# Optimization experiments

Measured on AMD Instinct MI355X. Metric: run time of the kernel, lower is better.

The kernel has to match this reference:

```python
import jax, jax.numpy as jnp
import numpy as np

NUM_HEADS = 16
HEAD_DIM = 64
NEG_INF = -1000000000.0


def rotary_embedding(x, seq_len, head_dim):
    # x: (batch, seq, heads, head_dim)
    positions = jnp.arange(seq_len)
    dim_pairs = jnp.arange(0, head_dim, 2)
    freqs = 1.0 / 10000.0 ** (dim_pairs / head_dim)
    angles = positions[:, None] * freqs[None, :]          # (seq, head_dim/2)
    cos = jnp.cos(angles)[:, None, :]                     # (seq, 1, head_dim/2) -> broadcast over heads
    sin = jnp.sin(angles)[:, None, :]
    x1 = x[..., ::2]
    x2 = x[..., 1::2]
    out1 = x1 * cos - x2 * sin
    out2 = x1 * sin + x2 * cos
    return jnp.stack([out1, out2], axis=-1).reshape(x.shape)


def setup_inputs() -> dict:
    key = jax.random.key(0)
    k1, k2, k3 = jax.random.split(key, 3)
    batch, seq_len, embed_dim = 2, 2048, 1024
    x = jax.random.normal(k1, (batch, seq_len, embed_dim), dtype=jnp.float32)
    W_qkv = jax.random.normal(k2, (embed_dim, 3 * NUM_HEADS * HEAD_DIM), dtype=jnp.float32) * 0.02
    W_out = jax.random.normal(k3, (NUM_HEADS * HEAD_DIM, embed_dim), dtype=jnp.float32) * 0.02
    return {"x": x, "W_qkv": W_qkv, "W_out": W_out}


def reference(x, W_qkv, W_out):
    batch, seq_len, embed_dim = x.shape
    qkv = jnp.einsum('bse,ef->bsf', x, W_qkv)
    qkv = qkv.reshape(batch, seq_len, 3, NUM_HEADS, HEAD_DIM)
    q, k, v = qkv[:, :, 0], qkv[:, :, 1], qkv[:, :, 2]
    q = rotary_embedding(q, seq_len, HEAD_DIM)
    k = rotary_embedding(k, seq_len, HEAD_DIM)
    scale = 1.0 / jnp.sqrt(jnp.asarray(HEAD_DIM, dtype=x.dtype))
    scores = jnp.einsum('bqhd,bkhd->bhqk', q, k) * scale   # (B,H,S,S)
    mask = jnp.tril(jnp.ones((seq_len, seq_len), dtype=bool))[None, None, :, :]
    scores = jnp.where(mask, scores, NEG_INF)
    weights = jax.nn.softmax(scores, axis=-1)
    out = jnp.einsum('bhqk,bkhd->bqhd', weights, v)
    out = out.reshape(batch, seq_len, NUM_HEADS * HEAD_DIM)
    return jnp.einsum('bsf,fe->bse', out, W_out)
```

## Files before the change

### kernel.cpp

```cpp
#include <hip/hip_runtime.h>
#include <hip/hip_bf16.h>

typedef __attribute__((ext_vector_type(8))) short short8;
typedef __attribute__((ext_vector_type(4))) float float4v;

__device__ inline short8 rope8(short8 raw, float4 tA, float4 tB, float scale) {
  float c[4] = {tA.x, tA.z, tB.x, tB.z};
  float s[4] = {tA.y, tA.w, tB.y, tB.w};
  union { short8 v; short e[8]; } in, out;
  in.v = raw;
  #pragma unroll
  for (int j = 0; j < 4; ++j) {
    __hip_bfloat16 h1 = *reinterpret_cast<__hip_bfloat16*>(&in.e[2 * j]);
    __hip_bfloat16 h2 = *reinterpret_cast<__hip_bfloat16*>(&in.e[2 * j + 1]);
    const float x1 = __bfloat162float(h1), x2 = __bfloat162float(h2);
    __hip_bfloat16 o1 = __float2bfloat16((x1 * c[j] - x2 * s[j]) * scale);
    __hip_bfloat16 o2 = __float2bfloat16((x1 * s[j] + x2 * c[j]) * scale);
    out.e[2 * j]     = *reinterpret_cast<short*>(&o1);
    out.e[2 * j + 1] = *reinterpret_cast<short*>(&o2);
  }
  return out.v;
}

__global__ __launch_bounds__(256) void prep_all(
    const float* __restrict__ x, __hip_bfloat16* __restrict__ xb,
    float2* __restrict__ tab,
    const float* __restrict__ Wqkv, const float* __restrict__ Wout,
    __hip_bfloat16* __restrict__ WqkvT, __hip_bfloat16* __restrict__ WoutT) {
  __shared__ __hip_bfloat16 tile[32][33];
  const int id = blockIdx.x;
  if (id < 4096) {
    const int i = id * 256 + threadIdx.x;
    const float4 v = *(const float4*)(x + (size_t)i * 4);
    __hip_bfloat16 o[4];
    o[0] = __float2bfloat16(v.x); o[1] = __float2bfloat16(v.y);
    o[2] = __float2bfloat16(v.z); o[3] = __float2bfloat16(v.w);
    *(uint2*)(xb + (size_t)i * 4) = *(const uint2*)o;
    return;
  }
  if (id < 4352) {
    const int i = (id - 4096) * 256 + threadIdx.x;
    const int s = i >> 5, p = i & 31;
    const float freq = powf(10000.f, -(float)(p * 2) / 64.f);
    float sn, cs;
    sincosf((float)s * freq, &sn, &cs);
    tab[i] = make_float2(cs, sn);
    return;
  }
  const float* in;
  __hip_bfloat16* out;
  int C, bx, by;
  if (id < 7424) {
    const int lid = id - 4352;
    in = Wqkv; out = WqkvT; C = 3072; bx = lid % 96; by = lid / 96;
  } else {
    const int lid = id - 7424;
    in = Wout; out = WoutT; C = 1024; bx = lid & 31; by = lid >> 5;
  }
  const int R = 1024;
  const int c0 = bx * 32, r0 = by * 32;
  const int tx = threadIdx.x & 31, ty = threadIdx.x >> 5;
  #pragma unroll
  for (int i = ty; i < 32; i += 8)
    tile[i][tx] = __float2bfloat16(in[(size_t)(r0 + i) * C + (c0 + tx)]);
  __syncthreads();
  const int sx = threadIdx.x & 15, sy = threadIdx.x >> 4;
  #pragma unroll
  for (int i = sy; i < 32; i += 16) {
    union { unsigned u; short e[2]; } pk;
    pk.e[0] = *reinterpret_cast<short*>(&tile[2 * sx][i]);
    pk.e[1] = *reinterpret_cast<short*>(&tile[2 * sx + 1][i]);
    *(unsigned*)&out[(size_t)(c0 + i) * R + r0 + 2 * sx] = pk.u;
  }
}

template <typename OutT, int BM, int BN>
__global__ __launch_bounds__(256) void gemm_bt(
    const __hip_bfloat16* __restrict__ A,
    const __hip_bfloat16* __restrict__ Bt,
    OutT* __restrict__ C,
    int M, int N, int K) {
  __shared__ __hip_bfloat16 lA[BM][64];
  __shared__ __hip_bfloat16 lB[BN][64];
  constexpr int NI = BM / 32, NJ = BN / 32;
  const int t = threadIdx.x;
  const int lane = t & 63, wave = t >> 6;
  const int quad = lane >> 4, ln = lane & 15;
  const int m0 = blockIdx.y * BM, n0 = blockIdx.x * BN;
  const int wm = (wave >> 1) * (BM / 2), wn = (wave & 1) * (BN / 2);
  const int srow = lane >> 3;
  const int schunk = ((lane & 7) ^ srow) * 8;

  float4v acc[NI][NJ];
  #pragma unroll
  for (int i = 0; i < NI; ++i)
    #pragma unroll
    for (int j = 0; j < NJ; ++j)
      acc[i][j] = (float4v){0.f, 0.f, 0.f, 0.f};

  for (int kt = 0; kt < K; kt += 64) {
    __syncthreads();
    #pragma unroll
    for (int g = 0; g < BM / 32; ++g) {
      const int rbase = wave * (BM / 4) + g * 8;
      __builtin_amdgcn_global_load_lds(
          (const __attribute__((address_space(1))) void*)
              (A + (size_t)(m0 + rbase + srow) * K + kt + schunk),
          (__attribute__((address_space(3))) void*)&lA[rbase][0], 16, 0, 0);
    }
    #pragma unroll
    for (int g = 0; g < BN / 32; ++g) {
      const int rbase = wave * (BN / 4) + g * 8;
      __builtin_amdgcn_global_load_lds(
          (const __attribute__((address_space(1))) void*)
              (Bt + (size_t)(n0 + rbase + srow) * K + kt + schunk),
          (__attribute__((address_space(3))) void*)&lB[rbase][0], 16, 0, 0);
    }
    __syncthreads();
    #pragma unroll
    for (int step = 0; step < 2; ++step) {
      short8 af[NI], bf[NJ];
      #pragma unroll
      for (int i = 0; i < NI; ++i)
        af[i] = *(const short8*)&lA[wm + i * 16 + ln][((step * 4 + quad) ^ (ln & 7)) * 8];
      #pragma unroll
      for (int j = 0; j < NJ; ++j)
        bf[j] = *(const short8*)&lB[wn + j * 16 + ln][((step * 4 + quad) ^ (ln & 7)) * 8];
      #pragma unroll
      for (int i = 0; i < NI; ++i)
        #pragma unroll
        for (int j = 0; j < NJ; ++j)
          acc[i][j] = __builtin_amdgcn_mfma_f32_16x16x32_bf16(af[i], bf[j], acc[i][j], 0, 0, 0);
    }
  }
  #pragma unroll
  for (int i = 0; i < NI; ++i)
    #pragma unroll
    for (int j = 0; j < NJ; ++j)
      #pragma unroll
      for (int r = 0; r < 4; ++r) {
        const int row = m0 + wm + i * 16 + quad * 4 + r;
        const int col = n0 + wn + j * 16 + ln;
        if constexpr (__is_same(OutT, float))
          C[(size_t)row * N + col] = acc[i][j][r];
        else
          C[(size_t)row * N + col] = __float2bfloat16(acc[i][j][r]);
      }
}

__global__ __launch_bounds__(256) void qkv_prep(
    const __hip_bfloat16* __restrict__ qkv,
    const float2* __restrict__ tab,
    __hip_bfloat16* __restrict__ K,
    __hip_bfloat16* __restrict__ Vt) {
  __shared__ __hip_bfloat16 tile[64][68];
  const int s0 = blockIdx.x * 64;
  const int bh = blockIdx.y;
  const int h = bh & 15, b = bh >> 4;
  const int t = threadIdx.x;

  const int dd = (t & 7) * 8;
  const int sl = t >> 3;
  #pragma unroll
  for (int ss = sl; ss < 64; ss += 32) {
    const int s = s0 + ss;
    short8 kv = *(const short8*)&qkv[(size_t)(b * 2048 + s) * 3072 + 1024 + h * 64 + dd];
    const float4 tA = *(const float4*)&tab[(size_t)s * 32 + (dd >> 1)];
    const float4 tB = *(const float4*)&tab[(size_t)s * 32 + (dd >> 1) + 2];
    *(short8*)&K[((size_t)bh * 2048 + s) * 64 + dd] = rope8(kv, tA, tB, 1.0f);
  }

  const int dgrp = (t & 15) * 4;
  const int srow = t >> 4;
  #pragma unroll
  for (int i = srow; i < 64; i += 16) {
    ushort4 v4 = *(const ushort4*)&qkv[(size_t)(b * 2048 + s0 + i) * 3072 + 2048 + h * 64 + dgrp];
    *(ushort4*)&tile[i][dgrp] = v4;
  }
  __syncthreads();
  const int vx = t & 15, vy = t >> 4;
  #pragma unroll
  for (int d = vy; d < 64; d += 16) {
    union { ushort4 v; short e[4]; } pk;
    #pragma unroll
    for (int jj = 0; jj < 4; ++jj)
      pk.e[jj] = *reinterpret_cast<short*>(&tile[4 * vx + jj][d]);
    *(ushort4*)&Vt[((size_t)bh * 64 + d) * 2048 + s0 + 4 * vx] = pk.v;
  }
}

__global__ __launch_bounds__(256) void attention(
    const __hip_bfloat16* __restrict__ qkv,
    const float2* __restrict__ tab,
    const __hip_bfloat16* __restrict__ K,
    const __hip_bfloat16* __restrict__ Vt,
    __hip_bfloat16* __restrict__ attn) {
  __shared__ __hip_bfloat16 lK[2][64][64];
  __shared__ __hip_bfloat16 lV[2][64][64];
  __shared__ __hip_bfloat16 lO[4][16][64];
  const int t = threadIdx.x;
  const int lane = t & 63, w = t >> 6;
  const int quad = lane >> 4, ln = lane & 15;
  const int id = blockIdx.x;
  const int bh = id & 31;
  const int j = id >> 5;
  const int k2 = j >> 3, g = j & 7;
  const int qt = 8 * k2 + ((k2 & 1) ? (7 - g) : g);
  const int q0 = qt * 64;
  const size_t base = (size_t)bh * 2048 * 64;
  const __hip_bfloat16* Kb = K + base;
  const __hip_bfloat16* Vb = Vt + base;
  const int b = bh >> 4, h = bh & 15;

  const int srow = lane >> 3;
  const int schunkV = ((lane & 7) ^ srow) * 8;
  const int rb0 = w * 16;
  const int sig_base = (ln >> 2) * 8 + (ln & 3);

  #pragma unroll
  for (int g2 = 0; g2 < 2; ++g2) {
    const int rbase = rb0 + g2 * 8;
    const int schunkK = (((lane & 7) ^ srow) ^ (g2 << 2)) * 8;
    __builtin_amdgcn_global_load_lds(
        (const __attribute__((address_space(1))) void*)
            (Kb + (size_t)(rbase + srow) * 64 + schunkK),
        (__attribute__((address_space(3))) void*)&lK[0][rbase][0], 16, 0, 0);
    __builtin_amdgcn_global_load_lds(
        (const __attribute__((address_space(1))) void*)
            (Vb + (size_t)(rbase + srow) * 2048 + schunkV),
        (__attribute__((address_space(3))) void*)&lV[0][rbase][0], 16, 0, 0);
  }

  short8 qf[2];
  {
    const float qs = 0.125f * 1.44269504088896340736f;
    const int s = q0 + w * 16 + ln;
    const size_t qrow = (size_t)(b * 2048 + s) * 3072 + h * 64;
    short8 raw0 = *(const short8*)&qkv[qrow + quad * 8];
    short8 raw1 = *(const short8*)&qkv[qrow + 32 + quad * 8];
    const float4 ta = *(const float4*)&tab[(size_t)s * 32 + quad * 4];
    const float4 tb = *(const float4*)&tab[(size_t)s * 32 + quad * 4 + 2];
    const float4 tc = *(const float4*)&tab[(size_t)s * 32 + 16 + quad * 4];
    const float4 td = *(const float4*)&tab[(size_t)s * 32 + 16 + quad * 4 + 2];
    qf[0] = rope8(raw0, ta, tb, qs);
    qf[1] = rope8(raw1, tc, td, qs);
  }

  float4v acc_o[4];
  #pragma unroll
  for (int dt = 0; dt < 4; ++dt) acc_o[dt] = (float4v){0.f, 0.f, 0.f, 0.f};
  float suml = 0.f;

  for (int kt = 0; kt <= qt; ++kt) {
    const int buf = kt & 1;
    __syncthreads();

    if (kt < qt) {
      #pragma unroll
      for (int g2 = 0; g2 < 2; ++g2) {
        const int rbase = rb0 + g2 * 8;
        const int schunkK = (((lane & 7) ^ srow) ^ (g2 << 2)) * 8;
        __builtin_amdgcn_global_load_lds(
            (const __attribute__((address_space(1))) void*)
                (Kb + (size_t)((kt + 1) * 64 + rbase + srow) * 64 + schunkK),
            (__attribute__((address_space(3))) void*)&lK[buf ^ 1][rbase][0], 16, 0, 0);
        __builtin_amdgcn_global_load_lds(
            (const __attribute__((address_space(1))) void*)
                (Vb + (size_t)(rbase + srow) * 2048 + (kt + 1) * 64 + schunkV),
            (__attribute__((address_space(3))) void*)&lV[buf ^ 1][rbase][0], 16, 0, 0);
      }
    }

    float4v s4[4];
    #pragma unroll
    for (int nt = 0; nt < 4; ++nt) {
      const int krow = sig_base + ((nt & 1) << 2) + ((nt >> 1) << 5);
      const int k7 = (krow & 7) ^ (((krow >> 3) & 1) << 2);
      float4v a = (float4v){0.f, 0.f, 0.f, 0.f};
      #pragma unroll
      for (int step = 0; step < 2; ++step) {
        short8 kf = *(const short8*)&lK[buf][krow][((step * 4 + quad) ^ k7) * 8];
        a = __builtin_amdgcn_mfma_f32_16x16x32_bf16(kf, qf[step], a, 0, 0, 0);
      }
      s4[nt] = a;
    }
    if (kt == qt) {
      const int qr = q0 + w * 16 + ln;
      #pragma unroll
      for (int nt = 0; nt < 4; ++nt)
        #pragma unroll
        for (int r = 0; r < 4; ++r) {
          const int kglob = kt * 64 + quad * 8 + ((nt & 1) << 2) + r + ((nt >> 1) << 5);
          if (kglob > qr) s4[nt][r] = -64.f;
        }
    }
    #pragma unroll
    for (int nt = 0; nt < 4; ++nt)
      #pragma unroll
      for (int r = 0; r < 4; ++r) {
        s4[nt][r] = __builtin_amdgcn_exp2f(s4[nt][r]);
        suml += s4[nt][r];
      }
    #pragma unroll
    for (int s = 0; s < 2; ++s) {
      union { short8 v; short e[8]; } pb;
      #pragma unroll
      for (int i = 0; i < 4; ++i) {
        __hip_bfloat16 b0 = __float2bfloat16(s4[2 * s][i]);
        __hip_bfloat16 b1 = __float2bfloat16(s4[2 * s + 1][i]);
        pb.e[i] = *reinterpret_cast<short*>(&b0);
        pb.e[4 + i] = *reinterpret_cast<short*>(&b1);
      }
      #pragma unroll
      for (int dt = 0; dt < 4; ++dt) {
        short8 vf = *(const short8*)&lV[buf][dt * 16 + ln][((s * 4 + quad) ^ (ln & 7)) * 8];
        acc_o[dt] = __builtin_amdgcn_mfma_f32_16x16x32_bf16(vf, pb.v, acc_o[dt], 0, 0, 0);
      }
    }
  }

  float l0 = suml + __shfl_xor(suml, 16);
  const float inv = 1.0f / (l0 + __shfl_xor(l0, 32));

  #pragma unroll
  for (int dt = 0; dt < 4; ++dt) {
    union { uint2 u; short e[4]; } pk;
    #pragma unroll
    for (int r = 0; r < 4; ++r) {
      __hip_bfloat16 bv = __float2bfloat16(acc_o[dt][r] * inv);
      pk.e[r] = *reinterpret_cast<short*>(&bv);
    }
    *(uint2*)&lO[w][ln][dt * 16 + quad * 4] = pk.u;
  }

  const int orow = lane >> 2;
  const int od = (lane & 3) * 16;
  const uint4 w0 = *(const uint4*)&lO[w][orow][od];
  const uint4 w1 = *(const uint4*)&lO[w][orow][od + 8];
  const size_t rg = (size_t)(b * 2048 + q0 + w * 16 + orow);
  *(uint4*)&attn[rg * 1024 + h * 64 + od] = w0;
  *(uint4*)&attn[rg * 1024 + h * 64 + od + 8] = w1;
}

extern "C" void kernel_launch(void* const* d_in, const int* in_sizes, int n_in,
                              void* d_out, int out_size, void* d_ws, size_t ws_size,
                              hipStream_t stream) {
  const float* x    = (const float*)d_in[0];
  const float* Wqkv = (const float*)d_in[1];
  const float* Wout = (const float*)d_in[2];
  float* out = (float*)d_out;

  __hip_bfloat16* ws = (__hip_bfloat16*)d_ws;
  __hip_bfloat16* xb    = ws;
  __hip_bfloat16* WqkvT = xb    + (size_t)4096 * 1024;
  __hip_bfloat16* WoutT = WqkvT + (size_t)3072 * 1024;
  __hip_bfloat16* qkv   = WoutT + (size_t)1024 * 1024;
  __hip_bfloat16* Q     = qkv   + (size_t)4096 * 3072;
  __hip_bfloat16* K     = Q     + (size_t)32 * 2048 * 64;
  __hip_bfloat16* Vt    = K     + (size_t)32 * 2048 * 64;
  __hip_bfloat16* attn  = Vt    + (size_t)32 * 2048 * 64;
  float2*         tab   = (float2*)(attn + (size_t)4096 * 1024);

  prep_all<<<8448, 256, 0, stream>>>(x, xb, tab, Wqkv, Wout, WqkvT, WoutT);
  gemm_bt<__hip_bfloat16, 128, 128><<<dim3(3072 / 128, 4096 / 128), 256, 0, stream>>>(xb, WqkvT, qkv, 4096, 3072, 1024);
  qkv_prep<<<dim3(32, 32), 256, 0, stream>>>(qkv, tab, K, Vt);
  attention<<<1024, 256, 0, stream>>>(qkv, tab, K, Vt, attn);
  gemm_bt<float, 128, 64><<<dim3(1024 / 64, 4096 / 128), 256, 0, stream>>>(attn, WoutT, out, 4096, 1024, 1024);
}
```

Before: 172.4 us.

## Replace QKV projection GEMM with 256x256 tile, 8-wave pipelined direct-to-LDS kernel

Swaps the generic 128x128 bf16 GEMM for the QKV projection with a dedicated 256x256-tile kernel using 512 threads. Global tiles are loaded straight into LDS with global_load_lds, double-buffered, using an XOR swizzle to avoid bank conflicts. Loads are staged in halves between four MFMA phases, with explicit vmcnt waits, barriers and setprio to overlap memory with compute. The launch is only 192 blocks, so fewer blocks than CUs, and the tighter synchronisation raises correctness risk and leaves some CUs idle.

```diff
diff --git a/kernel.cpp b/kernel.cpp
--- a/kernel.cpp
+++ b/kernel.cpp
@@ -3,6 +3,11 @@
 
 typedef __attribute__((ext_vector_type(8))) short short8;
 typedef __attribute__((ext_vector_type(4))) float float4v;
+
+#define VMC(N) do { asm volatile("s_waitcnt vmcnt(" #N ")" ::: "memory"); \
+                    __builtin_amdgcn_sched_barrier(0); } while (0)
+#define BAR()  do { __builtin_amdgcn_s_barrier(); \
+                    __builtin_amdgcn_sched_barrier(0); } while (0)
 
 __device__ inline short8 rope8(short8 raw, float4 tA, float4 tB, float scale) {
   float c[4] = {tA.x, tA.z, tB.x, tB.z};
@@ -145,6 +150,117 @@
           C[(size_t)row * N + col] = acc[i][j][r];
         else
           C[(size_t)row * N + col] = __float2bfloat16(acc[i][j][r]);
+      }
+}
+
+__global__ __launch_bounds__(512, 1) void gemm1_8p(
+    const __hip_bfloat16* __restrict__ A,
+    const __hip_bfloat16* __restrict__ Bt,
+    __hip_bfloat16* __restrict__ C) {
+  constexpr int KD = 1024, NN = 3072, NT = 16;
+  __shared__ __hip_bfloat16 lA[2][256][64];
+  __shared__ __hip_bfloat16 lB[2][256][64];
+  const int t = threadIdx.x;
+  const int lane = t & 63, w = t >> 6;
+  const int quad = lane >> 4, ln = lane & 15;
+  const int m0 = blockIdx.y * 256, n0 = blockIdx.x * 256;
+  const int wm = (w >> 2) * 128, wn = (w & 3) * 64;
+  const int srow = t >> 3;
+  const int dch = t & 7;
+
+  float4v acc[8][4];
+  #pragma unroll
+  for (int mq = 0; mq < 8; ++mq)
+    #pragma unroll
+    for (int nq = 0; nq < 4; ++nq)
+      acc[mq][nq] = (float4v){0.f, 0.f, 0.f, 0.f};
+
+  auto stageA = [&](int buf, int tile, int half) {
+    #pragma unroll
+    for (int g = 0; g < 2; ++g) {
+      const int row = g * 128 + half * 64 + srow;
+      const int gch = dch ^ (row & 7);
+      __builtin_amdgcn_global_load_lds(
+          (const __attribute__((address_space(1))) void*)
+              (A + (size_t)(m0 + row) * KD + tile * 64 + gch * 8),
+          (__attribute__((address_space(3))) void*)&lA[buf][row][dch * 8], 16, 0, 0);
+    }
+  };
+  auto stageB = [&](int buf, int tile, int half) {
+    #pragma unroll
+    for (int g = 0; g < 2; ++g) {
+      const int row = g * 128 + half * 32 + (srow & 31) + (srow >> 5) * 64;
+      const int gch = dch ^ (row & 7);
+      __builtin_amdgcn_global_load_lds(
+          (const __attribute__((address_space(1))) void*)
+              (Bt + (size_t)(n0 + row) * KD + tile * 64 + gch * 8),
+          (__attribute__((address_space(3))) void*)&lB[buf][row][dch * 8], 16, 0, 0);
+    }
+  };
+
+  short8 af[4][2];
+  auto loadA = [&](int buf, int ms) {
+    #pragma unroll
+    for (int mq = 0; mq < 4; ++mq) {
+      const int r = wm + ms * 64 + mq * 16 + ln;
+      #pragma unroll
+      for (int s = 0; s < 2; ++s)
+        af[mq][s] = *(const short8*)&lA[buf][r][((s * 4 + quad) ^ (r & 7)) * 8];
+    }
+  };
+  auto phase = [&](int buf, int ms, int ns) {
+    short8 bf[2][2];
+    #pragma unroll
+    for (int nq = 0; nq < 2; ++nq) {
+      const int r = wn + ns * 32 + nq * 16 + ln;
+      #pragma unroll
+      for (int s = 0; s < 2; ++s)
+        bf[nq][s] = *(const short8*)&lB[buf][r][((s * 4 + quad) ^ (r & 7)) * 8];
+    }
+    __builtin_amdgcn_s_setprio(1);
+    #pragma unroll
+    for (int s = 0; s < 2; ++s)
+      #pragma unroll
+      for (int mq = 0; mq < 4; ++mq)
+        #pragma unroll
+        for (int nq = 0; nq < 2; ++nq)
+          acc[ms * 4 + mq][ns * 2 + nq] = __builtin_amdgcn_mfma_f32_16x16x32_bf16(
+              af[mq][s], bf[nq][s], acc[ms * 4 + mq][ns * 2 + nq], 0, 0, 0);
+    __builtin_amdgcn_s_setprio(0);
+  };
+
+  stageA(0, 0, 0); stageB(0, 0, 0); stageA(0, 0, 1); stageB(0, 0, 1);
+  stageA(1, 1, 0); stageB(1, 1, 0);
+
+  for (int tile = 0; tile < NT; ++tile) {
+    const int buf = tile & 1;
+    if (tile < NT - 1) VMC(8); else VMC(4);
+    BAR();
+    if (tile + 1 < NT) stageA(buf ^ 1, tile + 1, 1);
+    loadA(buf, 0);
+    phase(buf, 0, 0);
+    if (tile < NT - 1) VMC(6); else VMC(0);
+    BAR();
+    if (tile + 1 < NT) stageB(buf ^ 1, tile + 1, 1);
+    phase(buf, 0, 1);
+    BAR();
+    if (tile + 2 < NT) stageA(buf, tile + 2, 0);
+    loadA(buf, 1);
+    phase(buf, 1, 0);
+    BAR();
+    if (tile + 2 < NT) stageB(buf, tile + 2, 0);
+    phase(buf, 1, 1);
+  }
+
+  #pragma unroll
+  for (int am = 0; am < 8; ++am)
+    #pragma unroll
+    for (int an = 0; an < 4; ++an)
+      #pragma unroll
+      for (int r = 0; r < 4; ++r) {
+        const int row = m0 + wm + (am >> 2) * 64 + (am & 3) * 16 + quad * 4 + r;
+        const int col = n0 + wn + (an >> 1) * 32 + (an & 1) * 16 + ln;
+        C[(size_t)row * NN + col] = __float2bfloat16(acc[am][an][r]);
       }
 }
 
@@ -362,7 +478,7 @@
   float2*         tab   = (float2*)(attn + (size_t)4096 * 1024);
 
   prep_all<<<8448, 256, 0, stream>>>(x, xb, tab, Wqkv, Wout, WqkvT, WoutT);
-  gemm_bt<__hip_bfloat16, 128, 128><<<dim3(3072 / 128, 4096 / 128), 256, 0, stream>>>(xb, WqkvT, qkv, 4096, 3072, 1024);
+  gemm1_8p<<<dim3(3072 / 256, 4096 / 256), 512, 0, stream>>>(xb, WqkvT, qkv);
   qkv_prep<<<dim3(32, 32), 256, 0, stream>>>(qkv, tab, K, Vt);
   attention<<<1024, 256, 0, stream>>>(qkv, tab, K, Vt, attn);
   gemm_bt<float, 128, 64><<<dim3(1024 / 64, 4096 / 128), 256, 0, stream>>>(attn, WoutT, out, 4096, 1024, 1024);
```

Result: slower. 188.9 us (+9.6%).

## Split long causal attention query tiles across two blocks with combine kernel

Applied to the files above, without the earlier changes.

Query tiles 16-31 now have their key range split in half across two blocks, each writing unnormalized fp32 partial outputs and row sums. A new combine kernel adds the partials, normalizes them, and writes bf16. This aims to cut the long-tail imbalance of causal attention, where late tiles do up to 32 iterations. In exchange it adds fp32 partial traffic, an extra launch, and drops the previous zigzag block ordering. The combine needs no max rescaling because the kernel already uses a fixed softmax offset.

```diff
diff --git a/kernel.cpp b/kernel.cpp
--- a/kernel.cpp
+++ b/kernel.cpp
@@ -194,7 +194,9 @@
     const float2* __restrict__ tab,
     const __hip_bfloat16* __restrict__ K,
     const __hip_bfloat16* __restrict__ Vt,
-    __hip_bfloat16* __restrict__ attn) {
+    __hip_bfloat16* __restrict__ attn,
+    float* __restrict__ Op,
+    float* __restrict__ lp) {
   __shared__ __hip_bfloat16 lK[2][64][64];
   __shared__ __hip_bfloat16 lV[2][64][64];
   __shared__ __hip_bfloat16 lO[4][16][64];
@@ -203,9 +205,12 @@
   const int quad = lane >> 4, ln = lane & 15;
   const int id = blockIdx.x;
   const int bh = id & 31;
-  const int j = id >> 5;
-  const int k2 = j >> 3, g = j & 7;
-  const int qt = 8 * k2 + ((k2 & 1) ? (7 - g) : g);
+  const int r = id >> 5;
+  int qt, lo, hi, half;
+  bool split;
+  if (r < 16)      { split = false; half = 0; qt = r;      lo = 0;             hi = qt + 1; }
+  else if (r < 32) { split = true;  half = 0; qt = r;      lo = 0;             hi = (qt + 2) >> 1; }
+  else             { split = true;  half = 1; qt = r - 16; lo = (qt + 2) >> 1; hi = qt + 1; }
   const int q0 = qt * 64;
   const size_t base = (size_t)bh * 2048 * 64;
   const __hip_bfloat16* Kb = K + base;
@@ -223,11 +228,11 @@
     const int schunkK = (((lane & 7) ^ srow) ^ (g2 << 2)) * 8;
     __builtin_amdgcn_global_load_lds(
         (const __attribute__((address_space(1))) void*)
-            (Kb + (size_t)(rbase + srow) * 64 + schunkK),
+            (Kb + (size_t)(lo * 64 + rbase + srow) * 64 + schunkK),
         (__attribute__((address_space(3))) void*)&lK[0][rbase][0], 16, 0, 0);
     __builtin_amdgcn_global_load_lds(
         (const __attribute__((address_space(1))) void*)
-            (Vb + (size_t)(rbase + srow) * 2048 + schunkV),
+            (Vb + (size_t)(rbase + srow) * 2048 + lo * 64 + schunkV),
         (__attribute__((address_space(3))) void*)&lV[0][rbase][0], 16, 0, 0);
   }
 
@@ -251,11 +256,11 @@
   for (int dt = 0; dt < 4; ++dt) acc_o[dt] = (float4v){0.f, 0.f, 0.f, 0.f};
   float suml = 0.f;
 
-  for (int kt = 0; kt <= qt; ++kt) {
-    const int buf = kt & 1;
+  for (int kt = lo; kt < hi; ++kt) {
+    const int buf = (kt - lo) & 1;
     __syncthreads();
 
-    if (kt < qt) {
+    if (kt + 1 < hi) {
       #pragma unroll
       for (int g2 = 0; g2 < 2; ++g2) {
         const int rbase = rb0 + g2 * 8;
@@ -289,17 +294,17 @@
       #pragma unroll
       for (int nt = 0; nt < 4; ++nt)
         #pragma unroll
-        for (int r = 0; r < 4; ++r) {
-          const int kglob = kt * 64 + quad * 8 + ((nt & 1) << 2) + r + ((nt >> 1) << 5);
-          if (kglob > qr) s4[nt][r] = -64.f;
+        for (int rr = 0; rr < 4; ++rr) {
+          const int kglob = kt * 64 + quad * 8 + ((nt & 1) << 2) + rr + ((nt >> 1) << 5);
+          if (kglob > qr) s4[nt][rr] = -64.f;
         }
     }
     #pragma unroll
     for (int nt = 0; nt < 4; ++nt)
       #pragma unroll
-      for (int r = 0; r < 4; ++r) {
-        s4[nt][r] = __builtin_amdgcn_exp2f(s4[nt][r]);
-        suml += s4[nt][r];
+      for (int rr = 0; rr < 4; ++rr) {
+        s4[nt][rr] = __builtin_amdgcn_exp2f(s4[nt][rr]);
+        suml += s4[nt][rr];
       }
     #pragma unroll
     for (int s = 0; s < 2; ++s) {
@@ -320,26 +325,57 @@
   }
 
   float l0 = suml + __shfl_xor(suml, 16);
-  const float inv = 1.0f / (l0 + __shfl_xor(l0, 32));
-
-  #pragma unroll
-  for (int dt = 0; dt < 4; ++dt) {
-    union { uint2 u; short e[4]; } pk;
-    #pragma unroll
-    for (int r = 0; r < 4; ++r) {
-      __hip_bfloat16 bv = __float2bfloat16(acc_o[dt][r] * inv);
-      pk.e[r] = *reinterpret_cast<short*>(&bv);
-    }
-    *(uint2*)&lO[w][ln][dt * 16 + quad * 4] = pk.u;
-  }
-
-  const int orow = lane >> 2;
-  const int od = (lane & 3) * 16;
-  const uint4 w0 = *(const uint4*)&lO[w][orow][od];
-  const uint4 w1 = *(const uint4*)&lO[w][orow][od + 8];
-  const size_t rg = (size_t)(b * 2048 + q0 + w * 16 + orow);
-  *(uint4*)&attn[rg * 1024 + h * 64 + od] = w0;
-  *(uint4*)&attn[rg * 1024 + h * 64 + od + 8] = w1;
+  const float lfull = l0 + __shfl_xor(l0, 32);
+
+  if (!split) {
+    const float inv = 1.0f / lfull;
+    #pragma unroll
+    for (int dt = 0; dt < 4; ++dt) {
+      union { uint2 u; short e[4]; } pk;
+      #pragma unroll
+      for (int rr = 0; rr < 4; ++rr) {
+        __hip_bfloat16 bv = __float2bfloat16(acc_o[dt][rr] * inv);
+        pk.e[rr] = *reinterpret_cast<short*>(&bv);
+      }
+      *(uint2*)&lO[w][ln][dt * 16 + quad * 4] = pk.u;
+    }
+    const int orow = lane >> 2;
+    const int od = (lane & 3) * 16;
+    const uint4 w0 = *(const uint4*)&lO[w][orow][od];
+    const uint4 w1 = *(const uint4*)&lO[w][orow][od + 8];
+    const size_t rg = (size_t)(b * 2048 + q0 + w * 16 + orow);
+    *(uint4*)&attn[rg * 1024 + h * 64 + od] = w0;
+    *(uint4*)&attn[rg * 1024 + h * 64 + od + 8] = w1;
+  } else {
+    const int qrel = (qt - 16) * 64 + w * 16 + ln;
+    const size_t rowoff = ((size_t)half * 32 + bh) * 1024 + qrel;
+    if (quad == 0) lp[rowoff] = lfull;
+    float* Ob = Op + rowoff * 64;
+    #pragma unroll
+    for (int dt = 0; dt < 4; ++dt)
+      *(float4v*)&Ob[dt * 16 + quad * 4] = acc_o[dt];
+  }
+}
+
+__global__ __launch_bounds__(256) void attn_combine(
+    const float* __restrict__ Op, const float* __restrict__ lp,
+    __hip_bfloat16* __restrict__ attn) {
+  const int i = blockIdx.x * 256 + threadIdx.x;
+  const int d4 = (i & 15) * 4;
+  const int srel = (i >> 4) & 1023;
+  const int bh = i >> 14;
+  const size_t rowoff = (size_t)bh * 1024 + srel;
+  const float l = lp[rowoff] + lp[(size_t)32 * 1024 + rowoff];
+  const float inv = 1.0f / l;
+  const float4 o0 = *(const float4*)&Op[rowoff * 64 + d4];
+  const float4 o1 = *(const float4*)&Op[(size_t)32 * 1024 * 64 + rowoff * 64 + d4];
+  const int b = bh >> 4, h = bh & 15, s = 1024 + srel;
+  __hip_bfloat16 o[4];
+  o[0] = __float2bfloat16((o0.x + o1.x) * inv);
+  o[1] = __float2bfloat16((o0.y + o1.y) * inv);
+  o[2] = __float2bfloat16((o0.z + o1.z) * inv);
+  o[3] = __float2bfloat16((o0.w + o1.w) * inv);
+  *(uint2*)&attn[((size_t)(b * 2048 + s)) * 1024 + h * 64 + d4] = *(const uint2*)o;
 }
 
 extern "C" void kernel_launch(void* const* d_in, const int* in_sizes, int n_in,
@@ -360,10 +396,13 @@
   __hip_bfloat16* Vt    = K     + (size_t)32 * 2048 * 64;
   __hip_bfloat16* attn  = Vt    + (size_t)32 * 2048 * 64;
   float2*         tab   = (float2*)(attn + (size_t)4096 * 1024);
+  float*          Op    = (float*)(tab + (size_t)2048 * 32);
+  float*          lp    = Op + (size_t)2 * 32 * 1024 * 64;
 
   prep_all<<<8448, 256, 0, stream>>>(x, xb, tab, Wqkv, Wout, WqkvT, WoutT);
   gemm_bt<__hip_bfloat16, 128, 128><<<dim3(3072 / 128, 4096 / 128), 256, 0, stream>>>(xb, WqkvT, qkv, 4096, 3072, 1024);
   qkv_prep<<<dim3(32, 32), 256, 0, stream>>>(qkv, tab, K, Vt);
-  attention<<<1024, 256, 0, stream>>>(qkv, tab, K, Vt, attn);
+  attention<<<1536, 256, 0, stream>>>(qkv, tab, K, Vt, attn, Op, lp);
+  attn_combine<<<2048, 256, 0, stream>>>(Op, lp, attn);
   gemm_bt<float, 128, 64><<<dim3(1024 / 64, 4096 / 128), 256, 0, stream>>>(attn, WoutT, out, 4096, 1024, 1024);
 }
```

Result: slower. 178.3 us (+3.5%).
